# Performance work log

Measured on AMD Instinct MI355X. Metric: run time of the kernel, lower is better.

Reference implementation:

```python
import jax, jax.numpy as jnp
import numpy as np

COMMITMENT_COST = 0.25
NUM_EMBEDDINGS = 1024
EMBEDDING_DIM = 256


def setup_inputs() -> dict:
    key = jax.random.key(0)
    k1, k2 = jax.random.split(key)
    inputs = jax.random.normal(k1, (32, 32, 32, EMBEDDING_DIM), dtype=jnp.float32)
    # GlorotUniform-ish init for the [D, K] codebook
    limit = float(np.sqrt(6.0 / (EMBEDDING_DIM + NUM_EMBEDDINGS)))
    w = jax.random.uniform(k2, (EMBEDDING_DIM, NUM_EMBEDDINGS), dtype=jnp.float32,
                           minval=-limit, maxval=limit)
    return {"inputs": inputs, "w": w}


def reference(inputs, w):
    D, K = w.shape
    flat = inputs.reshape(-1, D)                                   # [N, D]
    distances = (jnp.sum(flat * flat, axis=1, keepdims=True)
                 - 2.0 * (flat @ w)
                 + jnp.sum(w * w, axis=0, keepdims=True))          # [N, K]
    enc_idx_flat = jnp.argmin(distances, axis=1)                   # [N]
    encodings = jax.nn.one_hot(enc_idx_flat, K, dtype=inputs.dtype)  # [N, K]
    encoding_indices = enc_idx_flat.reshape(inputs.shape[:-1])     # [B, H, W]
    quantized = jnp.take(w.T, encoding_indices, axis=0)            # [B, H, W, D]

    e_latent_loss = jnp.mean((jax.lax.stop_gradient(quantized) - inputs) ** 2)
    q_latent_loss = jnp.mean((quantized - jax.lax.stop_gradient(inputs)) ** 2)
    loss = q_latent_loss + COMMITMENT_COST * e_latent_loss

    quantized_skip = inputs + jax.lax.stop_gradient(quantized - inputs)

    avg_probs = jnp.mean(encodings, axis=0)                        # [K]
    perplexity = jnp.exp(-jnp.sum(avg_probs * jnp.log(avg_probs + 1e-10)))
    return (quantized_skip, loss, perplexity, encodings, encoding_indices)
```

## Files before the change

kernel.cpp:

```cpp
#include <hip/hip_runtime.h>
#include <cfloat>
#include <cmath>
#include <stdint.h>

#define NROWS 32768
#define DIM   256
#define KC    1024

typedef short bf16x8 __attribute__((ext_vector_type(8)));
typedef float f32x4  __attribute__((ext_vector_type(4)));
typedef float f32x2  __attribute__((ext_vector_type(2)));

__device__ inline unsigned short f2bf(float f) {
    unsigned u = __float_as_uint(f);
    u = (u + 0x7fffu + ((u >> 16) & 1u)) >> 16;
    return (unsigned short)u;
}

__global__ __launch_bounds__(256) void prep_w(const float* __restrict__ w,
                                              uint4* __restrict__ wph,
                                              float* __restrict__ wT) {
    const int t = blockIdx.x * 256 + threadIdx.x;
    const int l = t & 63;
    const int ks = (t >> 6) & 7;
    const int ctg = t >> 9;
    const int c = ctg * 16 + (l & 15);
    const int kbase = ks * 32 + ((l >> 4) << 3);
    union { unsigned short u[8]; uint4 v; } H;
#pragma unroll
    for (int j = 0; j < 8; ++j) {
        float v = w[(size_t)(kbase + j) * KC + c];
        H.u[j] = f2bf(v);
        wT[(size_t)c * DIM + kbase + j] = v;
    }
    wph[t] = H.v;
}

__global__ __launch_bounds__(256) void wnorm_kernel(const float* __restrict__ wT,
                                                    double* __restrict__ wnorm64,
                                                    float* __restrict__ wnormf) {
    const int k = blockIdx.x * 256 + threadIdx.x;
    const float* p = wT + (size_t)k * DIM;
    double acc = 0.0;
#pragma unroll 8
    for (int d = 0; d < DIM; ++d) acc += (double)p[d] * (double)p[d];
    wnorm64[k] = acc;
    wnormf[k] = (float)acc;
}

__global__ __launch_bounds__(256, 4) void vq_screen(
    const float* __restrict__ x,
    const char* __restrict__ wph,
    const float* __restrict__ wnormf,
    int* __restrict__ cand)
{
    __shared__ char ldsbuf[32768];

    const int t = threadIdx.x;
    const int l = t & 63;
    const int wv = t >> 6;
    const int rowtile = blockIdx.x >> 1;
    const int p = blockIdx.x & 1;
    const int r0 = rowtile * 64 + wv * 16;
    const size_t pbase = (size_t)p * 262144;

    bf16x8 ah[8];
    {
        const float* xb = x + (size_t)(r0 + (l & 15)) * DIM + ((l >> 4) << 3);
#pragma unroll
        for (int ks = 0; ks < 8; ++ks) {
            float4 p0 = *(const float4*)(xb + ks * 32);
            float4 p1 = *(const float4*)(xb + ks * 32 + 4);
            float f[8] = {p0.x, p0.y, p0.z, p0.w, p1.x, p1.y, p1.z, p1.w};
            union { unsigned short u[8]; bf16x8 v; } H;
#pragma unroll
            for (int j = 0; j < 8; ++j) H.u[j] = f2bf(f[j]);
            ah[ks] = H.v;
        }
    }

    float tv0[4], tv1[4], tv2[4];
    int   tk0[4], tk1[4], tk2[4];
#pragma unroll
    for (int r = 0; r < 4; ++r) { tv0[r] = tv1[r] = tv2[r] = FLT_MAX; tk0[r] = tk1[r] = tk2[r] = 0; }

    {
        const char* g0 = wph + pbase + wv * 4096 + l * 16;
        char* lp0 = ldsbuf + wv * 4096 + l * 16;
#pragma unroll
        for (int i = 0; i < 4; ++i)
            __builtin_amdgcn_global_load_lds(
                (const __attribute__((address_space(1))) void*)(g0 + i * 1024),
                (__attribute__((address_space(3))) void*)(lp0 + i * 1024), 16, 0, 0);
    }
    __syncthreads();

    int cur = 0;
    for (int g = 0; g < 16; ++g) {
        if (g + 1 < 16) {
            const char* gp = wph + pbase + (size_t)(g + 1) * 16384 + wv * 4096 + l * 16;
            char* lp = ldsbuf + (cur ^ 1) * 16384 + wv * 4096 + l * 16;
#pragma unroll
            for (int i = 0; i < 4; ++i)
                __builtin_amdgcn_global_load_lds(
                    (const __attribute__((address_space(1))) void*)(gp + i * 1024),
                    (__attribute__((address_space(3))) void*)(lp + i * 1024), 16, 0, 0);
        }

        f32x4 acc[2];
#pragma unroll
        for (int ct = 0; ct < 2; ++ct) acc[ct] = (f32x4){0.f, 0.f, 0.f, 0.f};

#pragma unroll
        for (int ks = 0; ks < 8; ++ks) {
#pragma unroll
            for (int ct = 0; ct < 2; ++ct) {
                bf16x8 bh = *(const bf16x8*)(ldsbuf + cur * 16384 + ((ct * 8 + ks) * 64 + l) * 16);
                acc[ct] = __builtin_amdgcn_mfma_f32_16x16x32_bf16(ah[ks], bh, acc[ct], 0, 0, 0);
            }
        }

#pragma unroll
        for (int ct = 0; ct < 2; ++ct) {
            const int k = (p * 32 + g * 2 + ct) * 16 + (l & 15);
            const float wn = wnormf[k];
#pragma unroll
            for (int r = 0; r < 4; ++r) {
                float s = wn - 2.0f * acc[ct][r];
                if (s < tv2[r]) {
                    if (s < tv1[r]) {
                        tv2[r] = tv1[r]; tk2[r] = tk1[r];
                        if (s < tv0[r]) { tv1[r] = tv0[r]; tk1[r] = tk0[r]; tv0[r] = s; tk0[r] = k; }
                        else            { tv1[r] = s;      tk1[r] = k; }
                    } else { tv2[r] = s; tk2[r] = k; }
                }
            }
        }

        if (g + 1 < 16) __syncthreads();
        cur ^= 1;
    }

    float rowmin[4];
#pragma unroll
    for (int r = 0; r < 4; ++r) {
        float v = tv0[r];
#pragma unroll
        for (int m = 1; m <= 8; m <<= 1) v = fminf(v, __shfl_xor(v, m));
        rowmin[r] = v;
    }

    const float margin = 0.125f;
    const int grpShift = (l >> 4) * 16;
    const unsigned laneMask = (1u << (l & 15)) - 1u;
#pragma unroll
    for (int r = 0; r < 4; ++r) {
        const int row = r0 + ((l >> 4) << 2) + r;
        int* creg = cand + ((size_t)row * 2 + p) * 8;
        const float thr = rowmin[r] + margin;
        int base = 0;
        {
            bool c = tv0[r] <= thr;
            unsigned long long bal = __ballot(c);
            unsigned grp = (unsigned)(bal >> grpShift) & 0xFFFFu;
            int pos = base + __popc(grp & laneMask);
            if (c && pos < 7) creg[1 + pos] = tk0[r];
            base += __popc(grp);
        }
        {
            bool c = tv1[r] <= thr;
            unsigned long long bal = __ballot(c);
            unsigned grp = (unsigned)(bal >> grpShift) & 0xFFFFu;
            int pos = base + __popc(grp & laneMask);
            if (c && pos < 7) creg[1 + pos] = tk1[r];
            base += __popc(grp);
        }
        {
            bool c = tv2[r] <= thr;
            unsigned long long bal = __ballot(c);
            unsigned grp = (unsigned)(bal >> grpShift) & 0xFFFFu;
            int pos = base + __popc(grp & laneMask);
            if (c && pos < 7) creg[1 + pos] = tk2[r];
            base += __popc(grp);
        }
        if ((l & 15) == 0) creg[0] = base < 7 ? base : 7;
    }
}

__global__ __launch_bounds__(256) void vq_final(
    const float* __restrict__ x, const float* __restrict__ wT,
    const double* __restrict__ wnorm64,
    const int* __restrict__ cand,
    float* __restrict__ out_q, float* __restrict__ out_idx, float* __restrict__ out_enc,
    int* __restrict__ counts, double* __restrict__ loss_sum)
{
    const int t = threadIdx.x;
    const int l = t & 63;
    const int wv = t >> 6;
    __shared__ double wsum[4];

    double ls0 = 0.0, ls1 = 0.0, ls2 = 0.0, ls3 = 0.0;
    const int stride = gridDim.x * 4;
    for (int row = blockIdx.x * 4 + wv; row < NROWS; row += stride) {
        const float4 xv = ((const float4*)(x + (size_t)row * DIM))[l];

        const int* c0 = cand + (size_t)row * 16;
        double best = 1e300; int bk = 0x7FFFFFFF;
#pragma unroll
        for (int part = 0; part < 2; ++part) {
            const int* cp = c0 + part * 8;
            const int n = cp[0];
            for (int c = 0; c < n; ++c) {
                const int k = cp[1 + c];
                const float4 w4 = ((const float4*)(wT + (size_t)k * DIM))[l];
                double d = (double)xv.x * (double)w4.x;
                d = fma((double)xv.y, (double)w4.y, d);
                d = fma((double)xv.z, (double)w4.z, d);
                d = fma((double)xv.w, (double)w4.w, d);
#pragma unroll
                for (int m = 32; m > 0; m >>= 1) d += __shfl_xor(d, m);
                const double s = wnorm64[k] - 2.0 * d;
                if (s < best || (s == best && k < bk)) { best = s; bk = k; }
            }
        }
        const int k = __builtin_amdgcn_readfirstlane(bk);

        const float4 qv = ((const float4*)(wT + (size_t)k * DIM))[l];
        f32x4 o = {xv.x + (qv.x - xv.x), xv.y + (qv.y - xv.y),
                   xv.z + (qv.z - xv.z), xv.w + (qv.w - xv.w)};
        __builtin_nontemporal_store(o, (f32x4*)(out_q + (size_t)row * DIM) + l);
        double dx = (double)qv.x - (double)xv.x; ls0 = fma(dx, dx, ls0);
        dx = (double)qv.y - (double)xv.y; ls1 = fma(dx, dx, ls1);
        dx = (double)qv.z - (double)xv.z; ls2 = fma(dx, dx, ls2);
        dx = (double)qv.w - (double)xv.w; ls3 = fma(dx, dx, ls3);
        f32x2* er2 = (f32x2*)(out_enc + (size_t)row * KC);
        f32x2 z = {0.f, 0.f};
#pragma unroll
        for (int i = 0; i < 8; ++i)
            __builtin_nontemporal_store(z, er2 + i * 64 + l);
        if (l == ((k >> 1) & 63)) out_enc[(size_t)row * KC + k] = 1.0f;
        if (l == 0) {
            out_idx[row] = (float)k;
            atomicAdd(&counts[k], 1);
        }
    }
    double lsum = (ls0 + ls1) + (ls2 + ls3);
#pragma unroll
    for (int off = 32; off > 0; off >>= 1) lsum += __shfl_down(lsum, off);
    if (l == 0) wsum[wv] = lsum;
    __syncthreads();
    if (t == 0) atomicAdd(loss_sum, wsum[0] + wsum[1] + wsum[2] + wsum[3]);
}

__global__ __launch_bounds__(1024) void final_kernel(const int* __restrict__ counts,
                                                     const double* __restrict__ loss_sum,
                                                     float* __restrict__ out_loss,
                                                     float* __restrict__ out_ppl) {
    const int t = threadIdx.x;
    double p = (double)counts[t] * (1.0 / 32768.0);
    double term = -p * log(p + 1e-10);
#pragma unroll
    for (int off = 32; off > 0; off >>= 1) term += __shfl_down(term, off);
    __shared__ double ws[16];
    if ((t & 63) == 0) ws[t >> 6] = term;
    __syncthreads();
    if (t == 0) {
        double s = 0.0;
        for (int i = 0; i < 16; ++i) s += ws[i];
        *out_ppl = (float)exp(s);
        *out_loss = (float)(1.25 * loss_sum[0] * (1.0 / 8388608.0));
    }
}

extern "C" void kernel_launch(void* const* d_in, const int* in_sizes, int n_in,
                              void* d_out, int out_size, void* d_ws, size_t ws_size,
                              hipStream_t stream) {
    const float* x = (const float*)d_in[0];
    const float* w = (const float*)d_in[1];

    float* out = (float*)d_out;
    float* out_q    = out;
    float* out_loss = out + 8388608;
    float* out_ppl  = out + 8388609;
    float* out_enc  = out + 8388610;
    float* out_idx  = out + 8388610 + 33554432;

    char* wsb = (char*)d_ws;
    double* loss_sum = (double*)(wsb + 0);
    int*    counts   = (int*)(wsb + 64);
    double* wnorm64  = (double*)(wsb + 4160);
    float*  wnormf   = (float*)(wsb + 12352);
    float*  wT       = (float*)(wsb + 16448);
    uint4*  wph      = (uint4*)(wsb + 1065024);
    int*    cand     = (int*)(wsb + 1589312);

    (void)hipMemsetAsync(d_ws, 0, 4160, stream);

    prep_w<<<128, 256, 0, stream>>>(w, wph, wT);
    wnorm_kernel<<<4, 256, 0, stream>>>(wT, wnorm64, wnormf);
    vq_screen<<<1024, 256, 0, stream>>>(x, (const char*)wph, wnormf, cand);
    vq_final<<<2048, 256, 0, stream>>>(x, wT, wnorm64, cand,
                                       out_q, out_idx, out_enc, counts, loss_sum);
    final_kernel<<<1, 1024, 0, stream>>>(counts, loss_sum, out_loss, out_ppl);
}
```

Before: 138.4 us.

## Retile VQ screen to 32 rows per wave and skip fp64 rescoring for clear winners

The bf16 MFMA screening kernel now has each wave handle two 16-row A tiles, so every LDS codebook fragment feeds two MFMAs. The codebook is split into four partitions instead of two, and the occupancy hint drops from 4 to 3 blocks. The screen also writes each candidate's approximate score. The final kernel uses these scores to apply a global row threshold and runs the fp64 dot-product rescoring only when more than one candidate survives. This cuts LDS traffic per MFMA and most of the fp64 shuffle-reduction work, at the cost of higher register pressure, a larger candidate buffer, and reliance on the bf16 score margin for correctness.

```diff
diff --git a/kernel.cpp b/kernel.cpp
--- a/kernel.cpp
+++ b/kernel.cpp
@@ -48,7 +48,7 @@
     wnormf[k] = (float)acc;
 }
 
-__global__ __launch_bounds__(256, 4) void vq_screen(
+__global__ __launch_bounds__(256, 3) void vq_screen(
     const float* __restrict__ x,
     const char* __restrict__ wph,
     const float* __restrict__ wnormf,
@@ -59,14 +59,15 @@
     const int t = threadIdx.x;
     const int l = t & 63;
     const int wv = t >> 6;
-    const int rowtile = blockIdx.x >> 1;
-    const int p = blockIdx.x & 1;
-    const int r0 = rowtile * 64 + wv * 16;
-    const size_t pbase = (size_t)p * 262144;
-
-    bf16x8 ah[8];
-    {
-        const float* xb = x + (size_t)(r0 + (l & 15)) * DIM + ((l >> 4) << 3);
+    const int p = blockIdx.x & 3;
+    const int rt = blockIdx.x >> 2;
+    const int r0 = rt * 128 + wv * 32;
+    const size_t pbase = (size_t)p * 131072;
+
+    bf16x8 ah0[8], ah1[8];
+#pragma unroll
+    for (int s = 0; s < 2; ++s) {
+        const float* xb = x + (size_t)(r0 + s * 16 + (l & 15)) * DIM + ((l >> 4) << 3);
 #pragma unroll
         for (int ks = 0; ks < 8; ++ks) {
             float4 p0 = *(const float4*)(xb + ks * 32);
@@ -75,14 +76,14 @@
             union { unsigned short u[8]; bf16x8 v; } H;
 #pragma unroll
             for (int j = 0; j < 8; ++j) H.u[j] = f2bf(f[j]);
-            ah[ks] = H.v;
-        }
-    }
-
-    float tv0[4], tv1[4], tv2[4];
-    int   tk0[4], tk1[4], tk2[4];
-#pragma unroll
-    for (int r = 0; r < 4; ++r) { tv0[r] = tv1[r] = tv2[r] = FLT_MAX; tk0[r] = tk1[r] = tk2[r] = 0; }
+            if (s == 0) ah0[ks] = H.v; else ah1[ks] = H.v;
+        }
+    }
+
+    float tv0[8], tv1[8], tv2[8];
+    int   tk0[8], tk1[8], tk2[8];
+#pragma unroll
+    for (int s = 0; s < 8; ++s) { tv0[s] = tv1[s] = tv2[s] = FLT_MAX; tk0[s] = tk1[s] = tk2[s] = 0; }
 
     {
         const char* g0 = wph + pbase + wv * 4096 + l * 16;
@@ -96,8 +97,8 @@
     __syncthreads();
 
     int cur = 0;
-    for (int g = 0; g < 16; ++g) {
-        if (g + 1 < 16) {
+    for (int g = 0; g < 8; ++g) {
+        if (g + 1 < 8) {
             const char* gp = wph + pbase + (size_t)(g + 1) * 16384 + wv * 4096 + l * 16;
             char* lp = ldsbuf + (cur ^ 1) * 16384 + wv * 4096 + l * 16;
 #pragma unroll
@@ -107,80 +108,77 @@
                     (__attribute__((address_space(3))) void*)(lp + i * 1024), 16, 0, 0);
         }
 
-        f32x4 acc[2];
-#pragma unroll
-        for (int ct = 0; ct < 2; ++ct) acc[ct] = (f32x4){0.f, 0.f, 0.f, 0.f};
+        f32x4 acc[2][2];
+#pragma unroll
+        for (int ct = 0; ct < 2; ++ct)
+#pragma unroll
+            for (int s = 0; s < 2; ++s) acc[ct][s] = (f32x4){0.f, 0.f, 0.f, 0.f};
 
 #pragma unroll
         for (int ks = 0; ks < 8; ++ks) {
 #pragma unroll
             for (int ct = 0; ct < 2; ++ct) {
                 bf16x8 bh = *(const bf16x8*)(ldsbuf + cur * 16384 + ((ct * 8 + ks) * 64 + l) * 16);
-                acc[ct] = __builtin_amdgcn_mfma_f32_16x16x32_bf16(ah[ks], bh, acc[ct], 0, 0, 0);
+                acc[ct][0] = __builtin_amdgcn_mfma_f32_16x16x32_bf16(ah0[ks], bh, acc[ct][0], 0, 0, 0);
+                acc[ct][1] = __builtin_amdgcn_mfma_f32_16x16x32_bf16(ah1[ks], bh, acc[ct][1], 0, 0, 0);
             }
         }
 
 #pragma unroll
         for (int ct = 0; ct < 2; ++ct) {
-            const int k = (p * 32 + g * 2 + ct) * 16 + (l & 15);
+            const int k = (p * 16 + g * 2 + ct) * 16 + (l & 15);
             const float wn = wnormf[k];
 #pragma unroll
-            for (int r = 0; r < 4; ++r) {
-                float s = wn - 2.0f * acc[ct][r];
-                if (s < tv2[r]) {
-                    if (s < tv1[r]) {
-                        tv2[r] = tv1[r]; tk2[r] = tk1[r];
-                        if (s < tv0[r]) { tv1[r] = tv0[r]; tk1[r] = tk0[r]; tv0[r] = s; tk0[r] = k; }
-                        else            { tv1[r] = s;      tk1[r] = k; }
-                    } else { tv2[r] = s; tk2[r] = k; }
+            for (int s = 0; s < 8; ++s) {
+                float sc = fmaf(-2.0f, acc[ct][s >> 2][s & 3], wn);
+                if (sc < tv2[s]) {
+                    if (sc < tv1[s]) {
+                        tv2[s] = tv1[s]; tk2[s] = tk1[s];
+                        if (sc < tv0[s]) { tv1[s] = tv0[s]; tk1[s] = tk0[s]; tv0[s] = sc; tk0[s] = k; }
+                        else             { tv1[s] = sc;     tk1[s] = k; }
+                    } else { tv2[s] = sc; tk2[s] = k; }
                 }
             }
         }
 
-        if (g + 1 < 16) __syncthreads();
+        if (g + 1 < 8) __syncthreads();
         cur ^= 1;
-    }
-
-    float rowmin[4];
-#pragma unroll
-    for (int r = 0; r < 4; ++r) {
-        float v = tv0[r];
-#pragma unroll
-        for (int m = 1; m <= 8; m <<= 1) v = fminf(v, __shfl_xor(v, m));
-        rowmin[r] = v;
     }
 
     const float margin = 0.125f;
     const int grpShift = (l >> 4) * 16;
     const unsigned laneMask = (1u << (l & 15)) - 1u;
 #pragma unroll
-    for (int r = 0; r < 4; ++r) {
-        const int row = r0 + ((l >> 4) << 2) + r;
-        int* creg = cand + ((size_t)row * 2 + p) * 8;
-        const float thr = rowmin[r] + margin;
+    for (int s = 0; s < 8; ++s) {
+        float v = tv0[s];
+#pragma unroll
+        for (int m = 1; m <= 8; m <<= 1) v = fminf(v, __shfl_xor(v, m));
+        const float thr = v + margin;
+        const int row = r0 + (s >> 2) * 16 + ((l >> 4) << 2) + (s & 3);
+        int* creg = cand + ((size_t)row * 4 + p) * 16;
         int base = 0;
         {
-            bool c = tv0[r] <= thr;
+            bool c = tv0[s] <= thr;
             unsigned long long bal = __ballot(c);
             unsigned grp = (unsigned)(bal >> grpShift) & 0xFFFFu;
             int pos = base + __popc(grp & laneMask);
-            if (c && pos < 7) creg[1 + pos] = tk0[r];
+            if (c && pos < 7) { creg[1 + pos] = tk0[s]; creg[8 + pos] = __float_as_int(tv0[s]); }
             base += __popc(grp);
         }
         {
-            bool c = tv1[r] <= thr;
+            bool c = tv1[s] <= thr;
             unsigned long long bal = __ballot(c);
             unsigned grp = (unsigned)(bal >> grpShift) & 0xFFFFu;
             int pos = base + __popc(grp & laneMask);
-            if (c && pos < 7) creg[1 + pos] = tk1[r];
+            if (c && pos < 7) { creg[1 + pos] = tk1[s]; creg[8 + pos] = __float_as_int(tv1[s]); }
             base += __popc(grp);
         }
         {
-            bool c = tv2[r] <= thr;
+            bool c = tv2[s] <= thr;
             unsigned long long bal = __ballot(c);
             unsigned grp = (unsigned)(bal >> grpShift) & 0xFFFFu;
             int pos = base + __popc(grp & laneMask);
-            if (c && pos < 7) creg[1 + pos] = tk2[r];
+            if (c && pos < 7) { creg[1 + pos] = tk2[s]; creg[8 + pos] = __float_as_int(tv2[s]); }
             base += __popc(grp);
         }
         if ((l & 15) == 0) creg[0] = base < 7 ? base : 7;
@@ -198,29 +196,50 @@
     const int l = t & 63;
     const int wv = t >> 6;
     __shared__ double wsum[4];
+    const float margin = 0.125f;
 
     double ls0 = 0.0, ls1 = 0.0, ls2 = 0.0, ls3 = 0.0;
     const int stride = gridDim.x * 4;
     for (int row = blockIdx.x * 4 + wv; row < NROWS; row += stride) {
         const float4 xv = ((const float4*)(x + (size_t)row * DIM))[l];
-
-        const int* c0 = cand + (size_t)row * 16;
-        double best = 1e300; int bk = 0x7FFFFFFF;
-#pragma unroll
-        for (int part = 0; part < 2; ++part) {
-            const int* cp = c0 + part * 8;
+        const int* c0 = cand + (size_t)row * 64;
+
+        float m = FLT_MAX;
+#pragma unroll
+        for (int p4 = 0; p4 < 4; ++p4) {
+            const int* cp = c0 + p4 * 16;
             const int n = cp[0];
-            for (int c = 0; c < n; ++c) {
-                const int k = cp[1 + c];
-                const float4 w4 = ((const float4*)(wT + (size_t)k * DIM))[l];
-                double d = (double)xv.x * (double)w4.x;
-                d = fma((double)xv.y, (double)w4.y, d);
-                d = fma((double)xv.z, (double)w4.z, d);
-                d = fma((double)xv.w, (double)w4.w, d);
-#pragma unroll
-                for (int m = 32; m > 0; m >>= 1) d += __shfl_xor(d, m);
-                const double s = wnorm64[k] - 2.0 * d;
-                if (s < best || (s == best && k < bk)) { best = s; bk = k; }
+            for (int c = 0; c < n; ++c) m = fminf(m, __int_as_float(cp[8 + c]));
+        }
+        const float thr = m + margin;
+
+        int bk = 0x7FFFFFFF, cnt = 0;
+#pragma unroll
+        for (int p4 = 0; p4 < 4; ++p4) {
+            const int* cp = c0 + p4 * 16;
+            const int n = cp[0];
+            for (int c = 0; c < n; ++c)
+                if (__int_as_float(cp[8 + c]) <= thr) { ++cnt; bk = cp[1 + c]; }
+        }
+        if (cnt > 1) {
+            double best = 1e300; bk = 0x7FFFFFFF;
+#pragma unroll
+            for (int p4 = 0; p4 < 4; ++p4) {
+                const int* cp = c0 + p4 * 16;
+                const int n = cp[0];
+                for (int c = 0; c < n; ++c) {
+                    if (__int_as_float(cp[8 + c]) > thr) continue;
+                    const int k2 = cp[1 + c];
+                    const float4 w4 = ((const float4*)(wT + (size_t)k2 * DIM))[l];
+                    double d = (double)xv.x * (double)w4.x;
+                    d = fma((double)xv.y, (double)w4.y, d);
+                    d = fma((double)xv.z, (double)w4.z, d);
+                    d = fma((double)xv.w, (double)w4.w, d);
+#pragma unroll
+                    for (int mm = 32; mm > 0; mm >>= 1) d += __shfl_xor(d, mm);
+                    const double s64 = wnorm64[k2] - 2.0 * d;
+                    if (s64 < best || (s64 == best && k2 < bk)) { best = s64; bk = k2; }
+                }
             }
         }
         const int k = __builtin_amdgcn_readfirstlane(bk);
```

Measured after the change: 167.0 us. +20.7%, slower.

## Load codebook directly from global in screen, store scores to skip exact rescoring

Applied to the files above, without the earlier changes.

The screening kernel drops the double-buffered LDS staging and its barriers. Each wave now reads its bf16 codebook fragments straight from global/L2, one 16-column tile at a time. The screen also writes each candidate's approximate score next to its index, and the candidate buffer doubles in size. The final kernel builds a global threshold from those scores and skips the FP64 exact distance recompute when only one candidate survives, which cuts wT gathers and shuffle reductions. The risk is more global-load traffic and latency in the screen, plus a reliance on the bf16 margin for correctness in the skip path.

```diff
diff --git a/kernel.cpp b/kernel.cpp
--- a/kernel.cpp
+++ b/kernel.cpp
@@ -54,15 +54,13 @@
     const float* __restrict__ wnormf,
     int* __restrict__ cand)
 {
-    __shared__ char ldsbuf[32768];
-
     const int t = threadIdx.x;
     const int l = t & 63;
     const int wv = t >> 6;
-    const int rowtile = blockIdx.x >> 1;
     const int p = blockIdx.x & 1;
-    const int r0 = rowtile * 64 + wv * 16;
-    const size_t pbase = (size_t)p * 262144;
+    const int rt = blockIdx.x >> 1;
+    const int r0 = rt * 64 + wv * 16;
+    const char* wp = wph + (size_t)p * 262144;
 
     bf16x8 ah[8];
     {
@@ -84,70 +82,32 @@
 #pragma unroll
     for (int r = 0; r < 4; ++r) { tv0[r] = tv1[r] = tv2[r] = FLT_MAX; tk0[r] = tk1[r] = tk2[r] = 0; }
 
-    {
-        const char* g0 = wph + pbase + wv * 4096 + l * 16;
-        char* lp0 = ldsbuf + wv * 4096 + l * 16;
-#pragma unroll
-        for (int i = 0; i < 4; ++i)
-            __builtin_amdgcn_global_load_lds(
-                (const __attribute__((address_space(1))) void*)(g0 + i * 1024),
-                (__attribute__((address_space(3))) void*)(lp0 + i * 1024), 16, 0, 0);
-    }
-    __syncthreads();
-
-    int cur = 0;
-    for (int g = 0; g < 16; ++g) {
-        if (g + 1 < 16) {
-            const char* gp = wph + pbase + (size_t)(g + 1) * 16384 + wv * 4096 + l * 16;
-            char* lp = ldsbuf + (cur ^ 1) * 16384 + wv * 4096 + l * 16;
-#pragma unroll
-            for (int i = 0; i < 4; ++i)
-                __builtin_amdgcn_global_load_lds(
-                    (const __attribute__((address_space(1))) void*)(gp + i * 1024),
-                    (__attribute__((address_space(3))) void*)(lp + i * 1024), 16, 0, 0);
-        }
-
-        f32x4 acc[2];
-#pragma unroll
-        for (int ct = 0; ct < 2; ++ct) acc[ct] = (f32x4){0.f, 0.f, 0.f, 0.f};
-
-#pragma unroll
-        for (int ks = 0; ks < 8; ++ks) {
-#pragma unroll
-            for (int ct = 0; ct < 2; ++ct) {
-                bf16x8 bh = *(const bf16x8*)(ldsbuf + cur * 16384 + ((ct * 8 + ks) * 64 + l) * 16);
-                acc[ct] = __builtin_amdgcn_mfma_f32_16x16x32_bf16(ah[ks], bh, acc[ct], 0, 0, 0);
+#pragma unroll 2
+    for (int ctg = 0; ctg < 32; ++ctg) {
+        const char* bp = wp + (size_t)ctg * 8192 + l * 16;
+        bf16x8 b[8];
+#pragma unroll
+        for (int ks = 0; ks < 8; ++ks)
+            b[ks] = *(const bf16x8*)(bp + ks * 1024);
+
+        f32x4 acc = (f32x4){0.f, 0.f, 0.f, 0.f};
+#pragma unroll
+        for (int ks = 0; ks < 8; ++ks)
+            acc = __builtin_amdgcn_mfma_f32_16x16x32_bf16(ah[ks], b[ks], acc, 0, 0, 0);
+
+        const int k = (p * 32 + ctg) * 16 + (l & 15);
+        const float wn = wnormf[k];
+#pragma unroll
+        for (int r = 0; r < 4; ++r) {
+            float sc = fmaf(-2.0f, acc[r], wn);
+            if (sc < tv2[r]) {
+                if (sc < tv1[r]) {
+                    tv2[r] = tv1[r]; tk2[r] = tk1[r];
+                    if (sc < tv0[r]) { tv1[r] = tv0[r]; tk1[r] = tk0[r]; tv0[r] = sc; tk0[r] = k; }
+                    else             { tv1[r] = sc;     tk1[r] = k; }
+                } else { tv2[r] = sc; tk2[r] = k; }
             }
         }
-
-#pragma unroll
-        for (int ct = 0; ct < 2; ++ct) {
-            const int k = (p * 32 + g * 2 + ct) * 16 + (l & 15);
-            const float wn = wnormf[k];
-#pragma unroll
-            for (int r = 0; r < 4; ++r) {
-                float s = wn - 2.0f * acc[ct][r];
-                if (s < tv2[r]) {
-                    if (s < tv1[r]) {
-                        tv2[r] = tv1[r]; tk2[r] = tk1[r];
-                        if (s < tv0[r]) { tv1[r] = tv0[r]; tk1[r] = tk0[r]; tv0[r] = s; tk0[r] = k; }
-                        else            { tv1[r] = s;      tk1[r] = k; }
-                    } else { tv2[r] = s; tk2[r] = k; }
-                }
-            }
-        }
-
-        if (g + 1 < 16) __syncthreads();
-        cur ^= 1;
-    }
-
-    float rowmin[4];
-#pragma unroll
-    for (int r = 0; r < 4; ++r) {
-        float v = tv0[r];
-#pragma unroll
-        for (int m = 1; m <= 8; m <<= 1) v = fminf(v, __shfl_xor(v, m));
-        rowmin[r] = v;
     }
 
     const float margin = 0.125f;
@@ -155,16 +115,19 @@
     const unsigned laneMask = (1u << (l & 15)) - 1u;
 #pragma unroll
     for (int r = 0; r < 4; ++r) {
+        float v = tv0[r];
+#pragma unroll
+        for (int m = 1; m <= 8; m <<= 1) v = fminf(v, __shfl_xor(v, m));
+        const float thr = v + margin;
         const int row = r0 + ((l >> 4) << 2) + r;
-        int* creg = cand + ((size_t)row * 2 + p) * 8;
-        const float thr = rowmin[r] + margin;
+        int* creg = cand + ((size_t)row * 2 + p) * 16;
         int base = 0;
         {
             bool c = tv0[r] <= thr;
             unsigned long long bal = __ballot(c);
             unsigned grp = (unsigned)(bal >> grpShift) & 0xFFFFu;
             int pos = base + __popc(grp & laneMask);
-            if (c && pos < 7) creg[1 + pos] = tk0[r];
+            if (c && pos < 7) { creg[1 + pos] = tk0[r]; creg[8 + pos] = __float_as_int(tv0[r]); }
             base += __popc(grp);
         }
         {
@@ -172,7 +135,7 @@
             unsigned long long bal = __ballot(c);
             unsigned grp = (unsigned)(bal >> grpShift) & 0xFFFFu;
             int pos = base + __popc(grp & laneMask);
-            if (c && pos < 7) creg[1 + pos] = tk1[r];
+            if (c && pos < 7) { creg[1 + pos] = tk1[r]; creg[8 + pos] = __float_as_int(tv1[r]); }
             base += __popc(grp);
         }
         {
@@ -180,7 +143,7 @@
             unsigned long long bal = __ballot(c);
             unsigned grp = (unsigned)(bal >> grpShift) & 0xFFFFu;
             int pos = base + __popc(grp & laneMask);
-            if (c && pos < 7) creg[1 + pos] = tk2[r];
+            if (c && pos < 7) { creg[1 + pos] = tk2[r]; creg[8 + pos] = __float_as_int(tv2[r]); }
             base += __popc(grp);
         }
         if ((l & 15) == 0) creg[0] = base < 7 ? base : 7;
@@ -198,29 +161,50 @@
     const int l = t & 63;
     const int wv = t >> 6;
     __shared__ double wsum[4];
+    const float margin = 0.125f;
 
     double ls0 = 0.0, ls1 = 0.0, ls2 = 0.0, ls3 = 0.0;
     const int stride = gridDim.x * 4;
     for (int row = blockIdx.x * 4 + wv; row < NROWS; row += stride) {
         const float4 xv = ((const float4*)(x + (size_t)row * DIM))[l];
-
-        const int* c0 = cand + (size_t)row * 16;
-        double best = 1e300; int bk = 0x7FFFFFFF;
-#pragma unroll
-        for (int part = 0; part < 2; ++part) {
-            const int* cp = c0 + part * 8;
+        const int* c0 = cand + (size_t)row * 32;
+
+        float m = FLT_MAX;
+#pragma unroll
+        for (int p2 = 0; p2 < 2; ++p2) {
+            const int* cp = c0 + p2 * 16;
             const int n = cp[0];
-            for (int c = 0; c < n; ++c) {
-                const int k = cp[1 + c];
-                const float4 w4 = ((const float4*)(wT + (size_t)k * DIM))[l];
-                double d = (double)xv.x * (double)w4.x;
-                d = fma((double)xv.y, (double)w4.y, d);
-                d = fma((double)xv.z, (double)w4.z, d);
-                d = fma((double)xv.w, (double)w4.w, d);
-#pragma unroll
-                for (int m = 32; m > 0; m >>= 1) d += __shfl_xor(d, m);
-                const double s = wnorm64[k] - 2.0 * d;
-                if (s < best || (s == best && k < bk)) { best = s; bk = k; }
+            for (int c = 0; c < n; ++c) m = fminf(m, __int_as_float(cp[8 + c]));
+        }
+        const float thr = m + margin;
+
+        int bk = 0x7FFFFFFF, cnt = 0;
+#pragma unroll
+        for (int p2 = 0; p2 < 2; ++p2) {
+            const int* cp = c0 + p2 * 16;
+            const int n = cp[0];
+            for (int c = 0; c < n; ++c)
+                if (__int_as_float(cp[8 + c]) <= thr) { ++cnt; bk = cp[1 + c]; }
+        }
+        if (cnt > 1) {
+            double best = 1e300; bk = 0x7FFFFFFF;
+#pragma unroll
+            for (int p2 = 0; p2 < 2; ++p2) {
+                const int* cp = c0 + p2 * 16;
+                const int n = cp[0];
+                for (int c = 0; c < n; ++c) {
+                    if (__int_as_float(cp[8 + c]) > thr) continue;
+                    const int k2 = cp[1 + c];
+                    const float4 w4 = ((const float4*)(wT + (size_t)k2 * DIM))[l];
+                    double d = (double)xv.x * (double)w4.x;
+                    d = fma((double)xv.y, (double)w4.y, d);
+                    d = fma((double)xv.z, (double)w4.z, d);
+                    d = fma((double)xv.w, (double)w4.w, d);
+#pragma unroll
+                    for (int mm = 32; mm > 0; mm >>= 1) d += __shfl_xor(d, mm);
+                    const double s64 = wnorm64[k2] - 2.0 * d;
+                    if (s64 < best || (s64 == best && k2 < bk)) { best = s64; bk = k2; }
+                }
             }
         }
         const int k = __builtin_amdgcn_readfirstlane(bk);
```

Result: slower. 142.9 us (+3.2%).

## Zero one-hot output inside screen kernel and skip exact rescoring for clear winners

Applied to the files above, without the earlier changes.

The zero-fill of the large one-hot encodings buffer moves from the final kernel into the MFMA screening kernel. Each wave writes part of a row per codebook group, so those stores overlap with matrix compute instead of sitting in the bandwidth-bound final pass. The screen kernel now also saves its approximate bf16 scores alongside the candidate indices, and the cand layout doubles to hold them. The final kernel takes a global threshold across both halves and skips the fp64 rescoring when only one candidate is inside the margin. This saves gathers and shuffles for most rows, at the cost of trusting the bf16 margin and adding stores to the screen kernel.

```diff
diff --git a/kernel.cpp b/kernel.cpp
--- a/kernel.cpp
+++ b/kernel.cpp
@@ -52,16 +52,17 @@
     const float* __restrict__ x,
     const char* __restrict__ wph,
     const float* __restrict__ wnormf,
-    int* __restrict__ cand)
+    int* __restrict__ cand,
+    float* __restrict__ out_enc)
 {
     __shared__ char ldsbuf[32768];
 
     const int t = threadIdx.x;
     const int l = t & 63;
     const int wv = t >> 6;
-    const int rowtile = blockIdx.x >> 1;
     const int p = blockIdx.x & 1;
-    const int r0 = rowtile * 64 + wv * 16;
+    const int rt = blockIdx.x >> 1;
+    const int r0 = rt * 64 + wv * 16;
     const size_t pbase = (size_t)p * 262144;
 
     bf16x8 ah[8];
@@ -105,6 +106,15 @@
                 __builtin_amdgcn_global_load_lds(
                     (const __attribute__((address_space(1))) void*)(gp + i * 1024),
                     (__attribute__((address_space(3))) void*)(lp + i * 1024), 16, 0, 0);
+        }
+
+        {
+            const int zrow = r0 + g;
+            f32x2* er2 = (f32x2*)(out_enc + (size_t)zrow * KC + p * 512);
+            f32x2 z = {0.f, 0.f};
+#pragma unroll
+            for (int i = 0; i < 4; ++i)
+                __builtin_nontemporal_store(z, er2 + i * 64 + l);
         }
 
         f32x4 acc[2];
@@ -141,30 +151,24 @@
         cur ^= 1;
     }
 
-    float rowmin[4];
-#pragma unroll
-    for (int r = 0; r < 4; ++r) {
-        float v = tv0[r];
-#pragma unroll
-        for (int m = 1; m <= 8; m <<= 1) v = fminf(v, __shfl_xor(v, m));
-        rowmin[r] = v;
-    }
-
     const float margin = 0.125f;
     const int grpShift = (l >> 4) * 16;
     const unsigned laneMask = (1u << (l & 15)) - 1u;
 #pragma unroll
     for (int r = 0; r < 4; ++r) {
+        float v = tv0[r];
+#pragma unroll
+        for (int m = 1; m <= 8; m <<= 1) v = fminf(v, __shfl_xor(v, m));
+        const float thr = v + margin;
         const int row = r0 + ((l >> 4) << 2) + r;
-        int* creg = cand + ((size_t)row * 2 + p) * 8;
-        const float thr = rowmin[r] + margin;
+        int* creg = cand + ((size_t)row * 2 + p) * 16;
         int base = 0;
         {
             bool c = tv0[r] <= thr;
             unsigned long long bal = __ballot(c);
             unsigned grp = (unsigned)(bal >> grpShift) & 0xFFFFu;
             int pos = base + __popc(grp & laneMask);
-            if (c && pos < 7) creg[1 + pos] = tk0[r];
+            if (c && pos < 7) { creg[1 + pos] = tk0[r]; creg[8 + pos] = __float_as_int(tv0[r]); }
             base += __popc(grp);
         }
         {
@@ -172,7 +176,7 @@
             unsigned long long bal = __ballot(c);
             unsigned grp = (unsigned)(bal >> grpShift) & 0xFFFFu;
             int pos = base + __popc(grp & laneMask);
-            if (c && pos < 7) creg[1 + pos] = tk1[r];
+            if (c && pos < 7) { creg[1 + pos] = tk1[r]; creg[8 + pos] = __float_as_int(tv1[r]); }
             base += __popc(grp);
         }
         {
@@ -180,7 +184,7 @@
             unsigned long long bal = __ballot(c);
             unsigned grp = (unsigned)(bal >> grpShift) & 0xFFFFu;
             int pos = base + __popc(grp & laneMask);
-            if (c && pos < 7) creg[1 + pos] = tk2[r];
+            if (c && pos < 7) { creg[1 + pos] = tk2[r]; creg[8 + pos] = __float_as_int(tv2[r]); }
             base += __popc(grp);
         }
         if ((l & 15) == 0) creg[0] = base < 7 ? base : 7;
@@ -198,29 +202,50 @@
     const int l = t & 63;
     const int wv = t >> 6;
     __shared__ double wsum[4];
+    const float margin = 0.125f;
 
     double ls0 = 0.0, ls1 = 0.0, ls2 = 0.0, ls3 = 0.0;
     const int stride = gridDim.x * 4;
     for (int row = blockIdx.x * 4 + wv; row < NROWS; row += stride) {
         const float4 xv = ((const float4*)(x + (size_t)row * DIM))[l];
-
-        const int* c0 = cand + (size_t)row * 16;
-        double best = 1e300; int bk = 0x7FFFFFFF;
-#pragma unroll
-        for (int part = 0; part < 2; ++part) {
-            const int* cp = c0 + part * 8;
+        const int* c0 = cand + (size_t)row * 32;
+
+        float m = FLT_MAX;
+#pragma unroll
+        for (int p2 = 0; p2 < 2; ++p2) {
+            const int* cp = c0 + p2 * 16;
             const int n = cp[0];
-            for (int c = 0; c < n; ++c) {
-                const int k = cp[1 + c];
-                const float4 w4 = ((const float4*)(wT + (size_t)k * DIM))[l];
-                double d = (double)xv.x * (double)w4.x;
-                d = fma((double)xv.y, (double)w4.y, d);
-                d = fma((double)xv.z, (double)w4.z, d);
-                d = fma((double)xv.w, (double)w4.w, d);
-#pragma unroll
-                for (int m = 32; m > 0; m >>= 1) d += __shfl_xor(d, m);
-                const double s = wnorm64[k] - 2.0 * d;
-                if (s < best || (s == best && k < bk)) { best = s; bk = k; }
+            for (int c = 0; c < n; ++c) m = fminf(m, __int_as_float(cp[8 + c]));
+        }
+        const float thr = m + margin;
+
+        int bk = 0x7FFFFFFF, cnt = 0;
+#pragma unroll
+        for (int p2 = 0; p2 < 2; ++p2) {
+            const int* cp = c0 + p2 * 16;
+            const int n = cp[0];
+            for (int c = 0; c < n; ++c)
+                if (__int_as_float(cp[8 + c]) <= thr) { ++cnt; bk = cp[1 + c]; }
+        }
+        if (cnt > 1) {
+            double best = 1e300; bk = 0x7FFFFFFF;
+#pragma unroll
+            for (int p2 = 0; p2 < 2; ++p2) {
+                const int* cp = c0 + p2 * 16;
+                const int n = cp[0];
+                for (int c = 0; c < n; ++c) {
+                    if (__int_as_float(cp[8 + c]) > thr) continue;
+                    const int k2 = cp[1 + c];
+                    const float4 w4 = ((const float4*)(wT + (size_t)k2 * DIM))[l];
+                    double d = (double)xv.x * (double)w4.x;
+                    d = fma((double)xv.y, (double)w4.y, d);
+                    d = fma((double)xv.z, (double)w4.z, d);
+                    d = fma((double)xv.w, (double)w4.w, d);
+#pragma unroll
+                    for (int mm = 32; mm > 0; mm >>= 1) d += __shfl_xor(d, mm);
+                    const double s64 = wnorm64[k2] - 2.0 * d;
+                    if (s64 < best || (s64 == best && k2 < bk)) { best = s64; bk = k2; }
+                }
             }
         }
         const int k = __builtin_amdgcn_readfirstlane(bk);
@@ -233,13 +258,8 @@
         dx = (double)qv.y - (double)xv.y; ls1 = fma(dx, dx, ls1);
         dx = (double)qv.z - (double)xv.z; ls2 = fma(dx, dx, ls2);
         dx = (double)qv.w - (double)xv.w; ls3 = fma(dx, dx, ls3);
-        f32x2* er2 = (f32x2*)(out_enc + (size_t)row * KC);
-        f32x2 z = {0.f, 0.f};
-#pragma unroll
-        for (int i = 0; i < 8; ++i)
-            __builtin_nontemporal_store(z, er2 + i * 64 + l);
-        if (l == ((k >> 1) & 63)) out_enc[(size_t)row * KC + k] = 1.0f;
         if (l == 0) {
+            out_enc[(size_t)row * KC + k] = 1.0f;
             out_idx[row] = (float)k;
             atomicAdd(&counts[k], 1);
         }
@@ -298,7 +318,7 @@
 
     prep_w<<<128, 256, 0, stream>>>(w, wph, wT);
     wnorm_kernel<<<4, 256, 0, stream>>>(wT, wnorm64, wnormf);
-    vq_screen<<<1024, 256, 0, stream>>>(x, (const char*)wph, wnormf, cand);
+    vq_screen<<<1024, 256, 0, stream>>>(x, (const char*)wph, wnormf, cand, out_enc);
     vq_final<<<2048, 256, 0, stream>>>(x, wT, wnorm64, cand,
                                        out_q, out_idx, out_enc, counts, loss_sum);
     final_kernel<<<1, 1024, 0, stream>>>(counts, loss_sum, out_loss, out_ppl);
```

New measurement: 132.6 us. 4.2% less time.
